# Performance work log

Hardware: AMD Instinct MI355X
Metric: run time of the kernel (lower is better)

The kernel has to match this reference:

```python
import jax, jax.numpy as jnp
import numpy as np

LN_EPS = 1e-5


def layernorm(x, g, b):
    mu = jnp.mean(x, axis=-1, keepdims=True)
    var = jnp.mean((x - mu) ** 2, axis=-1, keepdims=True)
    return (x - mu) * jax.lax.rsqrt(var + LN_EPS) * g + b


def attention(x, qkv_w, proj_w, proj_b, num_heads):
    B, N, C = x.shape
    d = C // num_heads
    qkv = jnp.einsum('bnc,oc->bno', x, qkv_w)            # [B,N,3C], no bias (qkv_bias=False)
    qkv = qkv.reshape(B, N, num_heads, 3 * d).transpose(0, 2, 1, 3)  # [B,h,N,3d]
    q, k, v = qkv[..., :d], qkv[..., d:2 * d], qkv[..., 2 * d:]
    scores = jnp.einsum('bhnd,bhmd->bhnm', q, k) * (d ** -0.5)
    a = jax.nn.softmax(scores, axis=-1)
    o = jnp.einsum('bhnm,bhmd->bhnd', a, v).transpose(0, 2, 1, 3).reshape(B, N, C)
    return jnp.einsum('bnc,oc->bno', o, proj_w) + proj_b


def dwconv(x, w, b, H, W):
    # x: [B,N,C] -> NCHW depthwise 3x3 conv, stride 1, pad 1 -> [B,N,C]
    B, N, C = x.shape
    xi = x.transpose(0, 2, 1).reshape(B, C, H, W)
    y = jax.lax.conv_general_dilated(
        xi, w, window_strides=(1, 1), padding='SAME',
        dimension_numbers=('NCHW', 'OIHW', 'NCHW'), feature_group_count=C)
    y = y + b[None, :, None, None]
    return y.reshape(B, C, H * W).transpose(0, 2, 1)


def mlp(x, fc1_w, fc1_b, dw_w, dw_b, fc2_w, fc2_b, H, W):
    h = jnp.einsum('bnc,oc->bno', x, fc1_w) + fc1_b
    h = dwconv(h, dw_w, dw_b, H, W)
    h = jax.nn.gelu(h, approximate=False)  # torch nn.GELU default = exact erf
    return jnp.einsum('bnh,oh->bno', h, fc2_w) + fc2_b


def setup_inputs() -> dict:
    key = jax.random.key(0)
    ks = jax.random.split(key, 8)
    B, N, C, HID = 8, 1024, 512, 2048
    s = 0.02
    return {
        'x': jax.random.normal(ks[0], (B, N, C), jnp.float32),
        'ln1_g': jnp.ones((C,), jnp.float32),
        'ln1_b': jnp.zeros((C,), jnp.float32),
        'qkv_w': jax.random.normal(ks[1], (3 * C, C), jnp.float32) * s,
        'proj_w': jax.random.normal(ks[2], (C, C), jnp.float32) * s,
        'proj_b': jnp.zeros((C,), jnp.float32),
        'ln2_g': jnp.ones((C,), jnp.float32),
        'ln2_b': jnp.zeros((C,), jnp.float32),
        'fc1_w': jax.random.normal(ks[3], (HID, C), jnp.float32) * s,
        'fc1_b': jnp.zeros((HID,), jnp.float32),
        'dw_w': jax.random.normal(ks[4], (HID, 1, 3, 3), jnp.float32) * s,
        'dw_b': jnp.zeros((HID,), jnp.float32),
        'fc2_w': jax.random.normal(ks[5], (C, HID), jnp.float32) * s,
        'fc2_b': jnp.zeros((C,), jnp.float32),
        'H': 32,
        'W': 32,
    }


def reference(x, ln1_g, ln1_b, qkv_w, proj_w, proj_b, ln2_g, ln2_b,
              fc1_w, fc1_b, dw_w, dw_b, fc2_w, fc2_b, H, W):
    NUM_HEADS = 8
    x = x + attention(layernorm(x, ln1_g, ln1_b), qkv_w, proj_w, proj_b, NUM_HEADS)
    x = x + mlp(layernorm(x, ln2_g, ln2_b), fc1_w, fc1_b, dw_w, dw_b, fc2_w, fc2_b, H, W)
    return x
```

## Files before the change

kernel.cpp:

```cpp
#include <hip/hip_runtime.h>
#include <hip/hip_bf16.h>


typedef __attribute__((ext_vector_type(8))) short short8;
typedef __attribute__((ext_vector_type(4))) short s16x4;
typedef __attribute__((ext_vector_type(4))) float f32x4;

__device__ __forceinline__ float b2f(short s) {
    union { float f; unsigned u; } z; z.u = ((unsigned)(unsigned short)s) << 16; return z.f;
}
__device__ __forceinline__ short f2b(float f) {
    union { float f; unsigned u; } z; z.f = f;
    unsigned r = (z.u + 0x7fffu + ((z.u >> 16) & 1u)) >> 16;
    return (short)r;
}

__device__ __forceinline__ void gload_lds16(const void* g, void* l) {
    __builtin_amdgcn_global_load_lds(
        (const __attribute__((address_space(1))) void*)g,
        (__attribute__((address_space(3))) void*)l, 16, 0, 0);
}

__global__ __launch_bounds__(256) void cvt_weights(
    const float* __restrict__ s0, const float* __restrict__ s1,
    const float* __restrict__ s2, const float* __restrict__ s3,
    short* __restrict__ d0, short* __restrict__ d1,
    short* __restrict__ d2, short* __restrict__ d3) {
    long i = (long)blockIdx.x * 256 + threadIdx.x;
    const float* s; short* d; long off;
    if (i < 196608)      { s = s0; d = d0; off = i; }
    else if (i < 262144) { s = s1; d = d1; off = i - 196608; }
    else if (i < 524288) { s = s2; d = d2; off = i - 262144; }
    else                 { s = s3; d = d3; off = i - 524288; }
    float4 v = ((const float4*)s)[off];
    ushort4 o;
    o.x = (unsigned short)f2b(v.x); o.y = (unsigned short)f2b(v.y);
    o.z = (unsigned short)f2b(v.z); o.w = (unsigned short)f2b(v.w);
    ((ushort4*)d)[off] = o;
}

__global__ __launch_bounds__(256) void cvt_dw(
    const float* __restrict__ src, float* __restrict__ dst) {
    int i = blockIdx.x * 256 + threadIdx.x;
    int t = i >> 11, c = i & 2047;
    dst[t * 2048 + c] = src[c * 9 + t];
}

__global__ __launch_bounds__(256) void ln_kernel(
    const float* __restrict__ x, const float* __restrict__ g,
    const float* __restrict__ b, short* __restrict__ y) {
    int row  = blockIdx.x * 4 + (threadIdx.x >> 6);
    int lane = threadIdx.x & 63;
    const float* xr = x + (long)row * 512 + lane * 8;
    float4 v0 = ((const float4*)xr)[0];
    float4 v1 = ((const float4*)xr)[1];
    float e0[8] = {v0.x, v0.y, v0.z, v0.w, v1.x, v1.y, v1.z, v1.w};
    float s = 0.f;
#pragma unroll
    for (int e = 0; e < 8; e++) s += e0[e];
#pragma unroll
    for (int d = 1; d < 64; d <<= 1) s += __shfl_xor(s, d);
    float mu = s * (1.0f / 512.0f);
    float q = 0.f;
#pragma unroll
    for (int e = 0; e < 8; e++) { float t = e0[e] - mu; q += t * t; }
#pragma unroll
    for (int d = 1; d < 64; d <<= 1) q += __shfl_xor(q, d);
    float rs = rsqrtf(q * (1.0f / 512.0f) + 1e-5f);
    const float* gp = g + lane * 8;
    const float* bp = b + lane * 8;
    short8 o;
#pragma unroll
    for (int e = 0; e < 8; e++) o[e] = f2b((e0[e] - mu) * rs * gp[e] + bp[e]);
    *(short8*)(y + (long)row * 512 + lane * 8) = o;
}

template <int MT, typename Epi>
__global__ __launch_bounds__(256, 4) void gemm_bt(
    const short* __restrict__ A, const short* __restrict__ B, int K, Epi epi) {
    constexpr int NJ = (MT == 128) ? 4 : 2;
    __shared__ short As[MT * 64];
    __shared__ short Bs[128 * 64];
    int tid = threadIdx.x;
    int lane = tid & 63, w = tid >> 6;
    int lr = lane & 15, lq = lane >> 4;
    int wm = (MT == 128) ? (w & 1) * 64 : 0;
    int wn = (MT == 128) ? (w >> 1) * 64 : w * 32;
    long r0 = (long)blockIdx.x * MT, o0 = (long)blockIdx.y * 128;
    f32x4 acc[4][NJ];
#pragma unroll
    for (int i = 0; i < 4; i++)
#pragma unroll
        for (int j = 0; j < NJ; j++) acc[i][j] = (f32x4){0.f, 0.f, 0.f, 0.f};
    const short* Ab = A + r0 * K;
    const short* Bb = B + o0 * K;
    int srow = tid >> 3;
    int sc = ((tid & 7) ^ (srow & 7)) * 8;
    for (int k0 = 0; k0 < K; k0 += 64) {
#pragma unroll
        for (int m = 0; m < MT / 32; m++)
            gload_lds16(Ab + (long)(srow + m * 32) * K + k0 + sc,
                        As + m * 2048 + w * 512);
#pragma unroll
        for (int m = 0; m < 4; m++)
            gload_lds16(Bb + (long)(srow + m * 32) * K + k0 + sc,
                        Bs + m * 2048 + w * 512);
        __syncthreads();
#pragma unroll
        for (int ks = 0; ks < 2; ks++) {
            short8 af[4], bfr[NJ];
#pragma unroll
            for (int i = 0; i < 4; i++) {
                int row = wm + i * 16 + lr;
                int c = ks * 4 + lq;
                af[i] = *(const short8*)&As[row * 64 + ((c ^ (row & 7)) * 8)];
            }
#pragma unroll
            for (int j = 0; j < NJ; j++) {
                int row = wn + j * 16 + lr;
                int c = ks * 4 + lq;
                bfr[j] = *(const short8*)&Bs[row * 64 + ((c ^ (row & 7)) * 8)];
            }
#pragma unroll
            for (int i = 0; i < 4; i++)
#pragma unroll
                for (int j = 0; j < NJ; j++)
                    acc[i][j] = __builtin_amdgcn_mfma_f32_16x16x32_bf16(
                        af[i], bfr[j], acc[i][j], 0, 0, 0);
        }
        __syncthreads();
    }
#pragma unroll
    for (int i = 0; i < 4; i++)
#pragma unroll
        for (int j = 0; j < NJ; j++)
#pragma unroll
            for (int rg = 0; rg < 4; rg++)
                epi((int)(r0 + wm + i * 16 + lq * 4 + rg),
                    (int)(o0 + wn + j * 16 + lr), acc[i][j][rg]);
}

struct EpiQKV {
    short *q, *k, *vt;
    __device__ void operator()(int r, int o, float v) const {
        int b = r >> 10, n = r & 1023;
        int h = o / 192, j = o - h * 192;
        int bh = b * 8 + h;
        short bv = f2b(v);
        if (j < 64)        q[((long)bh * 1024 + n) * 64 + j] = bv;
        else if (j < 128)  k[((long)bh * 1024 + n) * 64 + (j - 64)] = bv;
        else               vt[((long)bh * 64 + (j - 128)) * 1024 + n] = bv;
    }
};
struct EpiProj {
    const float* pb; const float* x; float* x1;
    __device__ void operator()(int r, int o, float v) const {
        long idx = (long)r * 512 + o;
        x1[idx] = v + pb[o] + x[idx];
    }
};
struct EpiBias {
    const float* bias; short* out; int O;
    __device__ void operator()(int r, int o, float v) const {
        out[(long)r * O + o] = f2b(v + bias[o]);
    }
};
struct EpiFc2 {
    const float* bias; const float* x1; float* out;
    __device__ void operator()(int r, int o, float v) const {
        long idx = (long)r * 512 + o;
        out[idx] = v + bias[o] + x1[idx];
    }
};

__global__ __launch_bounds__(256, 2) void attn_kernel(
    const short* __restrict__ Q, const short* __restrict__ K,
    const short* __restrict__ Vt, short* __restrict__ out) {
    __shared__ __align__(16) char smem[53248];
    int bh = blockIdx.x, qb = blockIdx.y;
    int tid = threadIdx.x, w = tid >> 6, lane = tid & 63;
    int lr = lane & 15, lq = lane >> 4;
    short* Kt = (short*)(smem + w * 13312);
    short* Vl = (short*)(smem + w * 13312 + 4096);
    short* Pt = (short*)(smem + w * 13312 + 8192);
    short* Oshb = (short*)smem;
    float* Lsh  = (float*)(smem + 36864);

    const short* Qb = Q + ((long)bh * 1024 + qb * 64) * 64;
    const short* Kb = K + (long)bh * 1024 * 64;
    const short* Vb = Vt + (long)bh * 64 * 1024;

    short8 qf[4][2];
#pragma unroll
    for (int jt = 0; jt < 4; jt++)
#pragma unroll
        for (int ks = 0; ks < 2; ks++)
            qf[jt][ks] = *(const short8*)(Qb + (jt * 16 + lr) * 64 + ks * 32 + lq * 8);

    f32x4 oacc[4][4];
#pragma unroll
    for (int mt = 0; mt < 4; mt++)
#pragma unroll
        for (int dt = 0; dt < 4; dt++) oacc[mt][dt] = (f32x4){0.f, 0.f, 0.f, 0.f};
    float lsum[4] = {0.f, 0.f, 0.f, 0.f};

    for (int it = 0; it < 8; it++) {
        int n0 = w * 256 + it * 32;
#pragma unroll
        for (int i = 0; i < 4; i++) {
            int s = i * 64 + lane;
            int row = s >> 3, ch = (s & 7) ^ (row & 7);
            gload_lds16(Kb + (long)(n0 + row) * 64 + ch * 8, Kt + i * 512);
        }
#pragma unroll
        for (int i = 0; i < 4; i++) {
            int s = i * 64 + lane;
            int row = s >> 2, ch = s & 3;
            gload_lds16(Vb + (long)row * 1024 + n0 + ch * 8, Vl + i * 512);
        }
        asm volatile("s_waitcnt vmcnt(0)" ::: "memory");
        f32x4 sacc[2][4];
#pragma unroll
        for (int kt = 0; kt < 2; kt++)
#pragma unroll
            for (int jt = 0; jt < 4; jt++) sacc[kt][jt] = (f32x4){0.f, 0.f, 0.f, 0.f};
#pragma unroll
        for (int ks = 0; ks < 2; ks++)
#pragma unroll
            for (int kt = 0; kt < 2; kt++) {
                short8 ak = *(const short8*)&Kt[(kt * 16 + lr) * 64 +
                                                (((ks * 4 + lq) ^ (lr & 7)) * 8)];
#pragma unroll
                for (int jt = 0; jt < 4; jt++)
                    sacc[kt][jt] = __builtin_amdgcn_mfma_f32_16x16x32_bf16(
                        ak, qf[jt][ks], sacc[kt][jt], 0, 0, 0);
            }
#pragma unroll
        for (int kt = 0; kt < 2; kt++)
#pragma unroll
            for (int jt = 0; jt < 4; jt++) {
                s16x4 pv;
#pragma unroll
                for (int rg = 0; rg < 4; rg++) {
                    float e = __expf(sacc[kt][jt][rg] * 0.125f);
                    lsum[jt] += e;
                    pv[rg] = f2b(e);
                }
                *(s16x4*)&Pt[(jt * 16 + lr) * 40 + kt * 16 + lq * 4] = pv;
            }
        short8 bv[4];
#pragma unroll
        for (int dt = 0; dt < 4; dt++)
            bv[dt] = *(const short8*)&Vl[(dt * 16 + lr) * 32 + lq * 8];
#pragma unroll
        for (int mt = 0; mt < 4; mt++) {
            short8 ap = *(const short8*)&Pt[(mt * 16 + lr) * 40 + lq * 8];
#pragma unroll
            for (int dt = 0; dt < 4; dt++)
                oacc[mt][dt] = __builtin_amdgcn_mfma_f32_16x16x32_bf16(
                    ap, bv[dt], oacc[mt][dt], 0, 0, 0);
        }
    }
#pragma unroll
    for (int jt = 0; jt < 4; jt++) {
        lsum[jt] += __shfl_xor(lsum[jt], 16);
        lsum[jt] += __shfl_xor(lsum[jt], 32);
    }
    __syncthreads();
#pragma unroll
    for (int mt = 0; mt < 4; mt++)
#pragma unroll
        for (int dt = 0; dt < 4; dt++)
#pragma unroll
            for (int rg = 0; rg < 4; rg++)
                Oshb[w * 4608 + (mt * 16 + lq * 4 + rg) * 72 + dt * 16 + lr] =
                    f2b(oacc[mt][dt][rg]);
    if (lq == 0)
#pragma unroll
        for (int jt = 0; jt < 4; jt++) Lsh[w * 64 + jt * 16 + lr] = lsum[jt];
    __syncthreads();
    int m = tid >> 2, dg = (tid & 3) * 16;
    float l = Lsh[m] + Lsh[64 + m] + Lsh[128 + m] + Lsh[192 + m];
    float inv = 1.0f / l;
    float r[16];
#pragma unroll
    for (int i = 0; i < 16; i++) r[i] = 0.f;
#pragma unroll
    for (int ww = 0; ww < 4; ww++) {
        const short8* op = (const short8*)&Oshb[ww * 4608 + m * 72 + dg];
        short8 a = op[0], bq = op[1];
#pragma unroll
        for (int i = 0; i < 8; i++) { r[i] += b2f(a[i]); r[8 + i] += b2f(bq[i]); }
    }
    short8 o0, o1;
#pragma unroll
    for (int i = 0; i < 8; i++) { o0[i] = f2b(r[i] * inv); o1[i] = f2b(r[8 + i] * inv); }
    int b = bh >> 3, h = bh & 7;
    long base = ((long)(b * 1024 + qb * 64 + m)) * 512 + h * 64 + dg;
    *(short8*)(out + base) = o0;
    *(short8*)(out + base + 8) = o1;
}

__global__ __launch_bounds__(256) void dwconv_gelu(
    const short* __restrict__ h1, const float* __restrict__ wdT,
    const float* __restrict__ bias, short* __restrict__ h2) {
    int bn = blockIdx.x;
    int b = bn >> 10, n = bn & 1023;
    int yy = n >> 5, xx = n & 31;
    int c0 = threadIdx.x * 8;
    float4 bv0 = ((const float4*)&bias[c0])[0];
    float4 bv1 = ((const float4*)&bias[c0])[1];
    float acc[8] = {bv0.x, bv0.y, bv0.z, bv0.w, bv1.x, bv1.y, bv1.z, bv1.w};
    for (int ky = 0; ky < 3; ky++) {
        int ys = yy + ky - 1;
        if (ys < 0 || ys > 31) continue;
        for (int kx = 0; kx < 3; kx++) {
            int xs = xx + kx - 1;
            if (xs < 0 || xs > 31) continue;
            short8 hv = *(const short8*)&h1[((long)(b * 1024 + ys * 32 + xs)) * 2048 + c0];
            const float4* wp = (const float4*)&wdT[(ky * 3 + kx) * 2048 + c0];
            float4 wa = wp[0], wb = wp[1];
            float wv[8] = {wa.x, wa.y, wa.z, wa.w, wb.x, wb.y, wb.z, wb.w};
#pragma unroll
            for (int e = 0; e < 8; e++)
                acc[e] += b2f(hv[e]) * wv[e];
        }
    }
    short8 o;
#pragma unroll
    for (int e = 0; e < 8; e++) {
        float a = acc[e];
        o[e] = f2b(0.5f * a * (1.0f + erff(a * 0.70710678118f)));
    }
    *(short8*)&h2[((long)bn) * 2048 + c0] = o;
}

extern "C" void kernel_launch(void* const* d_in, const int* in_sizes, int n_in,
                              void* d_out, int out_size, void* d_ws, size_t ws_size,
                              hipStream_t stream) {
    const float* x      = (const float*)d_in[0];
    const float* ln1_g  = (const float*)d_in[1];
    const float* ln1_b  = (const float*)d_in[2];
    const float* qkv_w  = (const float*)d_in[3];
    const float* proj_w = (const float*)d_in[4];
    const float* proj_b = (const float*)d_in[5];
    const float* ln2_g  = (const float*)d_in[6];
    const float* ln2_b  = (const float*)d_in[7];
    const float* fc1_w  = (const float*)d_in[8];
    const float* fc1_b  = (const float*)d_in[9];
    const float* dw_w   = (const float*)d_in[10];
    const float* dw_b   = (const float*)d_in[11];
    const float* fc2_w  = (const float*)d_in[12];
    const float* fc2_b  = (const float*)d_in[13];
    float* out = (float*)d_out;

    char* p = (char*)d_ws;
    short* wq   = (short*)p; p += (long)1536 * 512 * 2;
    short* wp   = (short*)p; p += (long)512 * 512 * 2;
    short* w1   = (short*)p; p += (long)2048 * 512 * 2;
    short* w2   = (short*)p; p += (long)512 * 2048 * 2;
    float* wdT  = (float*)p; p += (long)9 * 2048 * 4;
    short* y1   = (short*)p; p += (long)8192 * 512 * 2;
    short* q    = (short*)p; p += (long)64 * 1024 * 64 * 2;
    short* k    = (short*)p; p += (long)64 * 1024 * 64 * 2;
    short* vt   = (short*)p; p += (long)64 * 64 * 1024 * 2;
    short* attn = (short*)p; p += (long)8192 * 512 * 2;
    float* x1   = (float*)p; p += (long)8192 * 512 * 4;
    short* y2   = (short*)p; p += (long)8192 * 512 * 2;
    short* h1   = (short*)p; p += (long)8192 * 2048 * 2;
    short* h2   = (short*)p; p += (long)8192 * 2048 * 2;
    if ((size_t)(p - (char*)d_ws) > ws_size) return;

    cvt_weights<<<3072, 256, 0, stream>>>(qkv_w, proj_w, fc1_w, fc2_w, wq, wp, w1, w2);
    cvt_dw<<<72, 256, 0, stream>>>(dw_w, wdT);
    ln_kernel<<<2048, 256, 0, stream>>>(x, ln1_g, ln1_b, y1);
    gemm_bt<128><<<dim3(64, 12), 256, 0, stream>>>(y1, wq, 512, EpiQKV{q, k, vt});
    attn_kernel<<<dim3(64, 16), 256, 0, stream>>>(q, k, vt, attn);
    gemm_bt<64><<<dim3(128, 4), 256, 0, stream>>>(attn, wp, 512,
                                                  EpiProj{proj_b, x, x1});
    ln_kernel<<<2048, 256, 0, stream>>>(x1, ln2_g, ln2_b, y2);
    gemm_bt<128><<<dim3(64, 16), 256, 0, stream>>>(y2, w1, 512,
                                                   EpiBias{fc1_b, h1, 2048});
    dwconv_gelu<<<8192, 256, 0, stream>>>(h1, wdT, dw_b, h2);
    gemm_bt<64><<<dim3(128, 4), 256, 0, stream>>>(h2, w2, 2048,
                                                  EpiFc2{fc2_b, x1, out});
}
```

Baseline: 286.8 us.

## Tile dwconv over 8-pixel row strips with sliding window and fast erf

The depthwise conv+GELU kernel now processes 8 consecutive pixels of a row per thread, keeping the 9 tap weights in registers and sliding a 3-column window so each input pixel is loaded once per row instead of up to three times. Exact erff is replaced with an Abramowitz-Stegun polynomial approximation. In attention, P is packed to bf16 by truncation instead of round-to-nearest, the P tile row stride drops from 40 to 36, and the occupancy hint is raised to 3 blocks per CU. These cut redundant loads and ALU work, at the cost of small precision loss in the GELU and the softmax weights.

```diff
diff --git a/kernel.cpp b/kernel.cpp
--- a/kernel.cpp
+++ b/kernel.cpp
@@ -13,6 +13,14 @@
     union { float f; unsigned u; } z; z.f = f;
     unsigned r = (z.u + 0x7fffu + ((z.u >> 16) & 1u)) >> 16;
     return (short)r;
+}
+__device__ __forceinline__ float erf_fast(float x) {
+    float ax = fabsf(x);
+    float t = 1.0f / fmaf(0.3275911f, ax, 1.0f);
+    float p = t * fmaf(t, fmaf(t, fmaf(t, fmaf(t, 1.061405429f, -1.453152027f),
+                        1.421413741f), -0.284496736f), 0.254829592f);
+    float r = 1.0f - p * __expf(-ax * ax);
+    return x < 0.f ? -r : r;
 }
 
 __device__ __forceinline__ void gload_lds16(const void* g, void* l) {
@@ -173,7 +181,7 @@
     }
 };
 
-__global__ __launch_bounds__(256, 2) void attn_kernel(
+__global__ __launch_bounds__(256, 3) void attn_kernel(
     const short* __restrict__ Q, const short* __restrict__ K,
     const short* __restrict__ Vt, short* __restrict__ out) {
     __shared__ __align__(16) char smem[53248];
@@ -239,14 +247,15 @@
         for (int kt = 0; kt < 2; kt++)
 #pragma unroll
             for (int jt = 0; jt < 4; jt++) {
-                s16x4 pv;
-#pragma unroll
-                for (int rg = 0; rg < 4; rg++) {
-                    float e = __expf(sacc[kt][jt][rg] * 0.125f);
-                    lsum[jt] += e;
-                    pv[rg] = f2b(e);
-                }
-                *(s16x4*)&Pt[(jt * 16 + lr) * 40 + kt * 16 + lq * 4] = pv;
+                float e0 = __expf(sacc[kt][jt][0] * 0.125f);
+                float e1 = __expf(sacc[kt][jt][1] * 0.125f);
+                float e2 = __expf(sacc[kt][jt][2] * 0.125f);
+                float e3 = __expf(sacc[kt][jt][3] * 0.125f);
+                lsum[jt] += (e0 + e1) + (e2 + e3);
+                uint2 pk;
+                pk.x = (__float_as_uint(e1) & 0xffff0000u) | (__float_as_uint(e0) >> 16);
+                pk.y = (__float_as_uint(e3) & 0xffff0000u) | (__float_as_uint(e2) >> 16);
+                *(uint2*)&Pt[(jt * 16 + lr) * 36 + kt * 16 + lq * 4] = pk;
             }
         short8 bv[4];
 #pragma unroll
@@ -254,7 +263,7 @@
             bv[dt] = *(const short8*)&Vl[(dt * 16 + lr) * 32 + lq * 8];
 #pragma unroll
         for (int mt = 0; mt < 4; mt++) {
-            short8 ap = *(const short8*)&Pt[(mt * 16 + lr) * 40 + lq * 8];
+            short8 ap = *(const short8*)&Pt[(mt * 16 + lr) * 36 + lq * 8];
 #pragma unroll
             for (int dt = 0; dt < 4; dt++)
                 oacc[mt][dt] = __builtin_amdgcn_mfma_f32_16x16x32_bf16(
@@ -301,38 +310,73 @@
     *(short8*)(out + base + 8) = o1;
 }
 
-__global__ __launch_bounds__(256) void dwconv_gelu(
+__global__ __launch_bounds__(256, 3) void dwconv_gelu(
     const short* __restrict__ h1, const float* __restrict__ wdT,
     const float* __restrict__ bias, short* __restrict__ h2) {
-    int bn = blockIdx.x;
-    int b = bn >> 10, n = bn & 1023;
-    int yy = n >> 5, xx = n & 31;
-    int c0 = threadIdx.x * 8;
-    float4 bv0 = ((const float4*)&bias[c0])[0];
-    float4 bv1 = ((const float4*)&bias[c0])[1];
-    float acc[8] = {bv0.x, bv0.y, bv0.z, bv0.w, bv1.x, bv1.y, bv1.z, bv1.w};
+    int ch = blockIdx.x & 1, xq = (blockIdx.x >> 1) & 3;
+    int yy = (blockIdx.x >> 3) & 31, b = blockIdx.x >> 8;
+    int c0 = ch * 1024 + threadIdx.x * 4;
+    int x0 = xq * 8;
+    float w[9][4];
+#pragma unroll
+    for (int t = 0; t < 9; t++) {
+        float4 v = *(const float4*)&wdT[t * 2048 + c0];
+        w[t][0] = v.x; w[t][1] = v.y; w[t][2] = v.z; w[t][3] = v.w;
+    }
+    float4 bv = *(const float4*)&bias[c0];
+    float acc[8][4];
+#pragma unroll
+    for (int xi = 0; xi < 8; xi++) {
+        acc[xi][0] = bv.x; acc[xi][1] = bv.y; acc[xi][2] = bv.z; acc[xi][3] = bv.w;
+    }
+#pragma unroll
     for (int ky = 0; ky < 3; ky++) {
         int ys = yy + ky - 1;
         if (ys < 0 || ys > 31) continue;
-        for (int kx = 0; kx < 3; kx++) {
-            int xs = xx + kx - 1;
-            if (xs < 0 || xs > 31) continue;
-            short8 hv = *(const short8*)&h1[((long)(b * 1024 + ys * 32 + xs)) * 2048 + c0];
-            const float4* wp = (const float4*)&wdT[(ky * 3 + kx) * 2048 + c0];
-            float4 wa = wp[0], wb = wp[1];
-            float wv[8] = {wa.x, wa.y, wa.z, wa.w, wb.x, wb.y, wb.z, wb.w};
-#pragma unroll
-            for (int e = 0; e < 8; e++)
-                acc[e] += b2f(hv[e]) * wv[e];
-        }
-    }
-    short8 o;
-#pragma unroll
-    for (int e = 0; e < 8; e++) {
-        float a = acc[e];
-        o[e] = f2b(0.5f * a * (1.0f + erff(a * 0.70710678118f)));
-    }
-    *(short8*)&h2[((long)bn) * 2048 + c0] = o;
+        const short* rp = h1 + ((long)(b * 1024 + ys * 32) * 2048 + c0);
+        float fa[4], fb[4], fc[4];
+        if (x0 > 0) {
+            s16x4 v = *(const s16x4*)(rp + (long)(x0 - 1) * 2048);
+#pragma unroll
+            for (int e = 0; e < 4; e++) fa[e] = b2f(v[e]);
+        } else {
+#pragma unroll
+            for (int e = 0; e < 4; e++) fa[e] = 0.f;
+        }
+        {
+            s16x4 v = *(const s16x4*)(rp + (long)x0 * 2048);
+#pragma unroll
+            for (int e = 0; e < 4; e++) fb[e] = b2f(v[e]);
+        }
+#pragma unroll
+        for (int xi = 0; xi < 8; xi++) {
+            int xs = x0 + xi + 1;
+            if (xs <= 31) {
+                s16x4 v = *(const s16x4*)(rp + (long)xs * 2048);
+#pragma unroll
+                for (int e = 0; e < 4; e++) fc[e] = b2f(v[e]);
+            } else {
+#pragma unroll
+                for (int e = 0; e < 4; e++) fc[e] = 0.f;
+            }
+#pragma unroll
+            for (int e = 0; e < 4; e++)
+                acc[xi][e] += fa[e] * w[ky * 3][e] + fb[e] * w[ky * 3 + 1][e] +
+                              fc[e] * w[ky * 3 + 2][e];
+#pragma unroll
+            for (int e = 0; e < 4; e++) { fa[e] = fb[e]; fb[e] = fc[e]; }
+        }
+    }
+#pragma unroll
+    for (int xi = 0; xi < 8; xi++) {
+        s16x4 o;
+#pragma unroll
+        for (int e = 0; e < 4; e++) {
+            float a = acc[xi][e];
+            o[e] = f2b(0.5f * a * (1.0f + erf_fast(a * 0.70710678118f)));
+        }
+        *(s16x4*)&h2[(long)(b * 1024 + yy * 32 + x0 + xi) * 2048 + c0] = o;
+    }
 }
 
 extern "C" void kernel_launch(void* const* d_in, const int* in_sizes, int n_in,
@@ -381,7 +425,7 @@
     ln_kernel<<<2048, 256, 0, stream>>>(x1, ln2_g, ln2_b, y2);
     gemm_bt<128><<<dim3(64, 16), 256, 0, stream>>>(y2, w1, 512,
                                                    EpiBias{fc1_b, h1, 2048});
-    dwconv_gelu<<<8192, 256, 0, stream>>>(h1, wdT, dw_b, h2);
+    dwconv_gelu<<<2048, 256, 0, stream>>>(h1, wdT, dw_b, h2);
     gemm_bt<64><<<dim3(128, 4), 256, 0, stream>>>(h2, w2, 2048,
                                                   EpiFc2{fc2_b, x1, out});
 }
```

Result: faster. 274.4 us (-4.3%).
